# Kernel tuning notes

Hardware: AMD Instinct MI355X
Metric: run time of the kernel (lower is better)

The kernel has to match this reference:

```python
import jax, jax.numpy as jnp
import numpy as np

EPS_NUMER = 1e-8   # numerator init in original code
EPS_D2 = 1e-12     # guard sqrt(0) on the (unused) diagonal


def setup_inputs() -> dict:
    key = jax.random.key(0)
    k0, k1, k2, k3 = jax.random.split(key, 4)
    B, T, C, H, W, D, NC = 128, 128, 3, 32, 32, 1024, 10
    data_t = jax.random.normal(k0, (B, T, 1, C, H, W), jnp.float32)
    responses_t = jax.random.normal(k1, (B, T, NC), jnp.float32)
    teaching_signal_t = jax.random.uniform(k2, (B, T, NC), jnp.float32)
    # feature extractor = single linear layer; scaled so distances are moderate
    W_fe = jax.random.normal(k3, (C * H * W, D), jnp.float32) / np.float32(np.sqrt(C * H * W))
    b_fe = jnp.zeros((D,), jnp.float32)
    c = jnp.ones((1,), jnp.float32)
    gamma = jnp.ones((1,), jnp.float32)
    return dict(responses_t=responses_t, data_t=data_t, teaching_signal_t=teaching_signal_t,
                W_fe=W_fe, b_fe=b_fe, c=c, gamma=gamma)


def reference(responses_t, data_t, teaching_signal_t, W_fe, b_fe, c, gamma):
    B, T = data_t.shape[:2]
    # feature extraction: (B*T, C*H*W) @ (C*H*W, D) -> (B, T, 1, D)
    x = data_t.reshape(B * T, -1)
    feats = (x @ W_fe + b_fe).reshape(B, T, 1, -1)
    f = feats[:, :, 0]                                   # (B, T, D)
    # batched pairwise euclidean distance, then extra .sqrt() as in original
    sq = jnp.sum(f * f, axis=-1)                          # (B, T)
    d2 = sq[:, :, None] + sq[:, None, :] - 2.0 * jnp.einsum('bsd,btd->bst', f, f)
    d2 = jnp.maximum(d2, EPS_D2)
    dist = jnp.sqrt(jnp.sqrt(d2))                         # sqrt(cdist) per original
    sims = jnp.exp(-c[0] * dist)                          # (B, S, T)
    # causal weighted sum: numers[b,t,cls] = eps + sum_{s<t} sims[b,s,t]*teach[b,s,cls]
    causal = jnp.tril(jnp.ones((T, T), sims.dtype), -1).T  # mask[s,t] = 1 if s < t
    numers = EPS_NUMER + jnp.einsum('bst,st,bsc->btc', sims, causal, teaching_signal_t)
    tmp = numers ** gamma[0]
    score = tmp / jnp.sum(tmp, axis=-1, keepdims=True)
    # t == 0 uses raw numers (all EPS_NUMER), not normalized
    score = score.at[:, 0].set(EPS_NUMER)
    responses = score[:, :, None, :]                      # (B, T, 1, NC)
    return responses
```

## Files before the change

kernel.cpp:

```cpp
#include <hip/hip_runtime.h>

typedef short short8 __attribute__((ext_vector_type(8)));
typedef float f32x4 __attribute__((ext_vector_type(4)));
typedef unsigned int uint4v __attribute__((ext_vector_type(4)));

#define EPS_NUMER_F 1e-8f
#define EPS_D2_F 1e-12f

#define BB 128
#define TT 128
#define DD 1024
#define CHW 3072
#define NC 10
#define MM (BB * TT)
#define NT 48

#define GLOAD_LDS16(g, l)                                              \
  __builtin_amdgcn_global_load_lds(                                    \
      (const __attribute__((address_space(1))) void*)(g),              \
      (__attribute__((address_space(3))) void*)(l), 16, 0, 0)

#define DS_READ_B128(dst_, off_) \
  asm volatile("ds_read_b128 %0, %1" : "=v"(dst_) : "v"(off_))
#define DS_WRITE_B128(off_, val_) \
  asm volatile("ds_write_b128 %0, %1" :: "v"(off_), "v"(val_))

#define GLB_LOAD_X4(dst_, voff_, imm_) \
  asm volatile("global_load_dwordx4 %0, %1, %2 offset:" #imm_ \
               : "=v"(dst_) : "v"(voff_), "s"(xbase))

static __device__ __forceinline__ unsigned lds_addr(const void* p) {
  return (unsigned)(unsigned long long)(const __attribute__((address_space(3))) void*)p;
}
static __device__ __forceinline__ unsigned cvt2(float lo, float hi) {
  unsigned r;
  asm("v_cvt_pk_bf16_f32 %0, %1, %2" : "=v"(r) : "v"(lo), "v"(hi));
  return r;
}

static __device__ __forceinline__ short f2bf(float x) {
  unsigned int u = __float_as_uint(x);
  u = (u + 0x7fffu + ((u >> 16) & 1u)) >> 16;
  return (short)u;
}
static __device__ __forceinline__ float bf2f(short x) {
  return __uint_as_float(((unsigned int)(unsigned short)x) << 16);
}

__global__ __launch_bounds__(256) void k_transpose_w(const float* __restrict__ W,
                                                     short* __restrict__ Wt) {
  __shared__ float tile[32][33];
  const int n0 = blockIdx.x * 32;
  const int k0 = blockIdx.y * 32;
  const int tx = threadIdx.x & 31;
  const int ty = threadIdx.x >> 5;
#pragma unroll
  for (int i = 0; i < 32; i += 8)
    tile[ty + i][tx] = W[(size_t)(k0 + ty + i) * DD + (n0 + tx)];
  __syncthreads();
#pragma unroll
  for (int i = 0; i < 32; i += 8)
    Wt[(size_t)(n0 + ty + i) * CHW + (k0 + tx)] = f2bf(tile[tx][ty + i]);
}

__global__ __launch_bounds__(512, 2) void k_gemm_8ph(const float* __restrict__ X,
                                                     const short* __restrict__ Wt,
                                                     const float* __restrict__ bias,
                                                     short* __restrict__ F) {
  __shared__ short As[2][256 * 64];
  __shared__ short Bs[2][256 * 64];

  const int bid = blockIdx.x;
  const int id = (bid & 7) * 32 + (bid >> 3);
  const int bm = (id >> 2) << 8;
  const int bn = (id & 3) << 8;

  const int tid = threadIdx.x;
  const int lane = tid & 63;
  const int wid = tid >> 6;
  const int wr = wid >> 2;
  const int wc = wid & 3;

  const int srow = lane >> 3;
  const int sslot = (lane & 7) ^ (lane >> 3);
  const short* bSrc = Wt + (size_t)(bn + srow) * CHW + sslot * 8;

#define STAGE_B_HALF(T_, h_) do {                                            \
    int base_ = (h_) * 128 + wid * 8;                                        \
    GLOAD_LDS16(bSrc + (size_t)(base_) * CHW + (T_) * 64,                    \
                &Bs[(T_) & 1][(base_) * 64]);                                \
    GLOAD_LDS16(bSrc + (size_t)(base_ + 64) * CHW + (T_) * 64,              \
                &Bs[(T_) & 1][(base_ + 64) * 64]);                           \
  } while (0)

  const int arow_st = wid * 16 + (lane >> 3);
  const unsigned long long xbase = (unsigned long long)X;
  unsigned voff[4];
#pragma unroll
  for (int h = 0; h < 2; ++h)
#pragma unroll
    for (int j = 0; j < 2; ++j)
      voff[h * 2 + j] = (unsigned)(((bm + h * 128 + j * 8 + arow_st) * (size_t)CHW
                                    + (lane & 7) * 8) * 4);
  const unsigned aposb = (unsigned)(((lane & 7) ^ (lane >> 3)) * 16);

  f32x4 ra[4], rb[4];

#define LOAD_A_H0() do {                                                     \
    GLB_LOAD_X4(ra[0], voff[0], 0);  GLB_LOAD_X4(ra[1], voff[0], 16);        \
    GLB_LOAD_X4(ra[2], voff[1], 0);  GLB_LOAD_X4(ra[3], voff[1], 16);        \
  } while (0)
#define LOAD_A_H1() do {                                                     \
    GLB_LOAD_X4(rb[0], voff[2], 0);  GLB_LOAD_X4(rb[1], voff[2], 16);        \
    GLB_LOAD_X4(rb[2], voff[3], 0);  GLB_LOAD_X4(rb[3], voff[3], 16);        \
  } while (0)
#define ADV_A() do { voff[0] += 256; voff[1] += 256; voff[2] += 256; voff[3] += 256; } while (0)
#define WRITE_A_HALF(T_, h_, d_) do {                                        \
    unsigned ad_ = aWrBase + (((T_) & 1) ? 32768u : 0u) + (h_) * 16384u;     \
    uint4v w0_, w1_;                                                         \
    w0_.x = cvt2(d_[0].x, d_[0].y); w0_.y = cvt2(d_[0].z, d_[0].w);          \
    w0_.z = cvt2(d_[1].x, d_[1].y); w0_.w = cvt2(d_[1].z, d_[1].w);          \
    DS_WRITE_B128(ad_, w0_);                                                 \
    w1_.x = cvt2(d_[2].x, d_[2].y); w1_.y = cvt2(d_[2].z, d_[2].w);          \
    w1_.z = cvt2(d_[3].x, d_[3].y); w1_.w = cvt2(d_[3].z, d_[3].w);          \
    DS_WRITE_B128(ad_ + 1024u, w1_);                                         \
  } while (0)

  const int fr = lane & 15;
  const int sl = lane >> 4;
  const int slotk0 = (0 + sl) ^ (lane & 7);
  const int slotk1 = (4 + sl) ^ (lane & 7);
  const int arow = wr * 128 + fr;
  const int brow = wc * 64 + fr;

  const unsigned aBase0 = lds_addr(&As[0][0]);
  const unsigned bBase0 = lds_addr(&Bs[0][0]);
  const unsigned aWrBase = aBase0 + (unsigned)(arow_st * 128) + aposb;

  f32x4 acc[8][4] = {};

  LOAD_A_H0();
  LOAD_A_H1();
  ADV_A();
  STAGE_B_HALF(0, 0); STAGE_B_HALF(0, 1);
  STAGE_B_HALF(1, 0); STAGE_B_HALF(1, 1);
  __builtin_amdgcn_sched_barrier(0);
  asm volatile("s_waitcnt vmcnt(4)");
  __builtin_amdgcn_sched_barrier(0);
  WRITE_A_HALF(0, 0, ra);
  WRITE_A_HALF(0, 1, rb);
  asm volatile("s_waitcnt lgkmcnt(0)");
  __builtin_amdgcn_sched_barrier(0);
  __builtin_amdgcn_s_barrier();

  for (int T = 0; T < NT; ++T) {
    const unsigned ab = aBase0 + ((T & 1) ? 32768u : 0u);
    const unsigned bb = bBase0 + ((T & 1) ? 32768u : 0u);
    short8 bf_[8];
    short8 aq[4];

#define READ_AQ(q_) do {                                                       \
      DS_READ_B128(aq[0], ab + (unsigned)((arow + (2*(q_))    *16)*128 + slotk0*16)); \
      DS_READ_B128(aq[1], ab + (unsigned)((arow + (2*(q_))    *16)*128 + slotk1*16)); \
      DS_READ_B128(aq[2], ab + (unsigned)((arow + (2*(q_) + 1)*16)*128 + slotk0*16)); \
      DS_READ_B128(aq[3], ab + (unsigned)((arow + (2*(q_) + 1)*16)*128 + slotk1*16)); \
    } while (0)
#define MFMA16(q_) do {                                                      \
      _Pragma("unroll")                                                      \
      for (int m2 = 0; m2 < 2; ++m2)                                         \
        _Pragma("unroll")                                                    \
        for (int ks = 0; ks < 2; ++ks)                                       \
          _Pragma("unroll")                                                  \
          for (int ni = 0; ni < 4; ++ni)                                     \
            acc[2*(q_)+m2][ni] = __builtin_amdgcn_mfma_f32_16x16x32_bf16(    \
                aq[m2*2+ks], bf_[ni*2+ks], acc[2*(q_)+m2][ni], 0, 0, 0);     \
    } while (0)
#define PHASE_MID() do {                                                     \
      __builtin_amdgcn_sched_barrier(0);                                     \
      __builtin_amdgcn_s_barrier();                                          \
      asm volatile("s_waitcnt lgkmcnt(0)");                                  \
      __builtin_amdgcn_sched_barrier(0);                                     \
    } while (0)

    if (T + 1 < NT) LOAD_A_H0();
#pragma unroll
    for (int ni = 0; ni < 4; ++ni) {
      DS_READ_B128(bf_[ni * 2 + 0], bb + (unsigned)((brow + ni * 16) * 128 + slotk0 * 16));
      DS_READ_B128(bf_[ni * 2 + 1], bb + (unsigned)((brow + ni * 16) * 128 + slotk1 * 16));
    }
    READ_AQ(0);
    PHASE_MID();
    __builtin_amdgcn_s_setprio(1);
    MFMA16(0);
    __builtin_amdgcn_s_setprio(0);
    __builtin_amdgcn_s_barrier();

    if (T + 1 < NT) LOAD_A_H1();
    ADV_A();
    READ_AQ(1);
    PHASE_MID();
    __builtin_amdgcn_s_setprio(1);
    MFMA16(1);
    __builtin_amdgcn_s_setprio(0);
    __builtin_amdgcn_s_barrier();

    READ_AQ(2);
    if (T + 2 < NT) {
      STAGE_B_HALF(T + 2, 0);
      __builtin_amdgcn_sched_barrier(0);
      asm volatile("s_waitcnt vmcnt(6)");
      __builtin_amdgcn_sched_barrier(0);
    } else if (T + 1 < NT) {
      __builtin_amdgcn_sched_barrier(0);
      asm volatile("s_waitcnt vmcnt(4)");
      __builtin_amdgcn_sched_barrier(0);
    }
    if (T + 1 < NT) WRITE_A_HALF(T + 1, 0, ra);
    PHASE_MID();
    __builtin_amdgcn_s_setprio(1);
    MFMA16(2);
    __builtin_amdgcn_s_setprio(0);
    __builtin_amdgcn_s_barrier();

    READ_AQ(3);
    if (T + 2 < NT) {
      STAGE_B_HALF(T + 2, 1);
      __builtin_amdgcn_sched_barrier(0);
      asm volatile("s_waitcnt vmcnt(4)");
      __builtin_amdgcn_sched_barrier(0);
    } else if (T + 1 < NT) {
      __builtin_amdgcn_sched_barrier(0);
      asm volatile("s_waitcnt vmcnt(0)");
      __builtin_amdgcn_sched_barrier(0);
    }
    if (T + 1 < NT) WRITE_A_HALF(T + 1, 1, rb);
    PHASE_MID();
    __builtin_amdgcn_s_setprio(1);
    MFMA16(3);
    __builtin_amdgcn_s_setprio(0);
    __builtin_amdgcn_s_barrier();
  }

  const int cc = lane & 15;
  const int crr = sl << 2;
#pragma unroll
  for (int ni = 0; ni < 4; ++ni) {
    int col = bn + wc * 64 + ni * 16 + cc;
    float bv = bias[col];
#pragma unroll
    for (int mi = 0; mi < 8; ++mi) {
      int row0 = bm + wr * 128 + mi * 16 + crr;
#pragma unroll
      for (int q = 0; q < 4; ++q)
        F[(size_t)(row0 + q) * DD + col] = f2bf(acc[mi][ni][q] + bv);
    }
  }
#undef READ_AQ
#undef MFMA16
#undef PHASE_MID
#undef STAGE_B_HALF
}

__global__ __launch_bounds__(256) void k_batch_sims(const short* __restrict__ F,
                                                    const float* __restrict__ teach,
                                                    const float* __restrict__ cptr,
                                                    const float* __restrict__ gptr,
                                                    float* __restrict__ out) {
  __shared__ short ftile[128][40];
  __shared__ float simsT[64][129];
  __shared__ float sqv[128];
  __shared__ float sqp[256];
  __shared__ float teach_s[128][NC];
  __shared__ float numer[64][NC];
  __shared__ float rsum[64];

  const int b = blockIdx.x >> 1;
  const int half = blockIdx.x & 1;
  const int tid = threadIdx.x;
  const int lane = tid & 63;
  const int w = tid >> 6;
  const size_t fbase = (size_t)b * TT * DD;

  for (int idx = tid; idx < TT * NC; idx += 256)
    teach_s[idx / NC][idx % NC] = teach[(size_t)b * TT * NC + idx];

  {
    int row = tid >> 1;
    int kh = (tid & 1) << 9;
    const short* fp = F + fbase + (size_t)row * DD + kh;
    float s = 0.f;
    for (int k = 0; k < 512; k += 8) {
      short8 v = *reinterpret_cast<const short8*>(fp + k);
#pragma unroll
      for (int j = 0; j < 8; ++j) { float x = bf2f(v[j]); s += x * x; }
    }
    sqp[tid] = s;
  }
  __syncthreads();
  if (tid < 128) sqv[tid] = sqp[2 * tid] + sqp[2 * tid + 1];
  __syncthreads();

  f32x4 acc[2][4] = {};
  const int fr = lane & 15;
  const int fk = (lane >> 4) << 3;
  for (int k0 = 0; k0 < DD; k0 += 32) {
#pragma unroll
    for (int i = 0; i < 2; ++i) {
      int idx = tid + (i << 8);
      int row = idx >> 2;
      int kc = (idx & 3) << 3;
      short8 v = *reinterpret_cast<const short8*>(F + fbase + (size_t)row * DD + (k0 + kc));
      *reinterpret_cast<short8*>(&ftile[row][kc]) = v;
    }
    __syncthreads();
    short8 af[2], bfv[4];
#pragma unroll
    for (int mi = 0; mi < 2; ++mi)
      af[mi] = *reinterpret_cast<const short8*>(&ftile[w * 32 + mi * 16 + fr][fk]);
#pragma unroll
    for (int ni = 0; ni < 4; ++ni)
      bfv[ni] = *reinterpret_cast<const short8*>(&ftile[half * 64 + ni * 16 + fr][fk]);
#pragma unroll
    for (int mi = 0; mi < 2; ++mi)
#pragma unroll
      for (int ni = 0; ni < 4; ++ni)
        acc[mi][ni] = __builtin_amdgcn_mfma_f32_16x16x32_bf16(af[mi], bfv[ni], acc[mi][ni], 0, 0, 0);
    __syncthreads();
  }

  const float c0 = cptr[0];
  const int cc = lane & 15;
  const int crr = (lane >> 4) << 2;
#pragma unroll
  for (int mi = 0; mi < 2; ++mi) {
#pragma unroll
    for (int ni = 0; ni < 4; ++ni) {
#pragma unroll
      for (int q = 0; q < 4; ++q) {
        int s_g = w * 32 + mi * 16 + crr + q;
        int tl = ni * 16 + cc;
        int t_g = half * 64 + tl;
        float g = acc[mi][ni][q];
        float d2 = sqv[s_g] + sqv[t_g] - 2.0f * g;
        d2 = fmaxf(d2, EPS_D2_F);
        float dist = sqrtf(sqrtf(d2));
        simsT[tl][s_g] = (s_g < t_g) ? expf(-c0 * dist) : 0.0f;
      }
    }
  }
  __syncthreads();

  const float gam = gptr[0];
  for (int idx = tid; idx < 64 * NC; idx += 256) {
    int tl = idx / NC, c = idx % NC;
    float s = 0.f;
#pragma unroll 4
    for (int si = 0; si < TT; ++si)
      s += simsT[tl][si] * teach_s[si][c];
    float v = EPS_NUMER_F + s;
    numer[tl][c] = (gam == 1.0f) ? v : powf(v, gam);
  }
  __syncthreads();
  if (tid < 64) {
    float s = 0.f;
#pragma unroll
    for (int c = 0; c < NC; ++c) s += numer[tid][c];
    rsum[tid] = s;
  }
  __syncthreads();
  for (int idx = tid; idx < 64 * NC; idx += 256) {
    int tl = idx / NC, c = idx % NC;
    int t_g = half * 64 + tl;
    float v = numer[tl][c] / rsum[tl];
    if (t_g == 0) v = EPS_NUMER_F;
    out[(size_t)b * TT * NC + (size_t)t_g * NC + c] = v;
  }
}

extern "C" void kernel_launch(void* const* d_in, const int* in_sizes, int n_in,
                              void* d_out, int out_size, void* d_ws, size_t ws_size,
                              hipStream_t stream) {
  const float* data = (const float*)d_in[1];
  const float* teach = (const float*)d_in[2];
  const float* Wfe = (const float*)d_in[3];
  const float* bfe = (const float*)d_in[4];
  const float* cp = (const float*)d_in[5];
  const float* gp = (const float*)d_in[6];
  float* outp = (float*)d_out;

  char* ws = (char*)d_ws;
  short* Wt = (short*)ws;
  short* F = (short*)(ws + (size_t)8 * 1024 * 1024);

  k_transpose_w<<<dim3(DD / 32, CHW / 32), 256, 0, stream>>>(Wfe, Wt);
  k_gemm_8ph<<<dim3((MM / 256) * (DD / 256)), 512, 0, stream>>>(data, Wt, bfe, F);
  k_batch_sims<<<dim3(BB * 2), 256, 0, stream>>>(F, teach, cp, gp, outp);
}
```

Baseline: 146.7 us.

## Double-buffer A fragments in registers to overlap LDS reads with MFMA

The feature-extraction GEMM main loop now keeps two register sets for A fragments (even and odd quarters). Each quarter's LDS reads are issued before the previous quarter's MFMAs, and the full lgkmcnt(0) waits become partial lgkmcnt waits. This is meant to hide LDS read latency behind matrix-core work instead of stalling at every phase boundary. In exchange it needs about 16 more VGPRs and relies on exact counts of outstanding LDS operations, which makes the code more fragile to ordering changes.

```diff
diff --git a/kernel.cpp b/kernel.cpp
--- a/kernel.cpp
+++ b/kernel.cpp
@@ -24,10 +24,10 @@
   asm volatile("ds_read_b128 %0, %1" : "=v"(dst_) : "v"(off_))
 #define DS_WRITE_B128(off_, val_) \
   asm volatile("ds_write_b128 %0, %1" :: "v"(off_), "v"(val_))
-
 #define GLB_LOAD_X4(dst_, voff_, imm_) \
   asm volatile("global_load_dwordx4 %0, %1, %2 offset:" #imm_ \
                : "=v"(dst_) : "v"(voff_), "s"(xbase))
+#define SCHED_FENCE() __builtin_amdgcn_sched_barrier(0)
 
 static __device__ __forceinline__ unsigned lds_addr(const void* p) {
   return (unsigned)(unsigned long long)(const __attribute__((address_space(3))) void*)p;
@@ -137,107 +137,125 @@
   const unsigned bBase0 = lds_addr(&Bs[0][0]);
   const unsigned aWrBase = aBase0 + (unsigned)(arow_st * 128) + aposb;
 
+  short8 bf_[8];
+  short8 aqE[4], aqO[4];
   f32x4 acc[8][4] = {};
+
+#define READ_B8(bb_) do {                                                    \
+    _Pragma("unroll")                                                        \
+    for (int ni = 0; ni < 4; ++ni) {                                         \
+      DS_READ_B128(bf_[ni * 2 + 0], (bb_) + (unsigned)((brow + ni * 16) * 128 + slotk0 * 16)); \
+      DS_READ_B128(bf_[ni * 2 + 1], (bb_) + (unsigned)((brow + ni * 16) * 128 + slotk1 * 16)); \
+    }                                                                        \
+  } while (0)
+#define READ_AQ(set_, q_, ab_) do {                                          \
+    DS_READ_B128(set_[0], (ab_) + (unsigned)((arow + (2*(q_))    *16)*128 + slotk0*16)); \
+    DS_READ_B128(set_[1], (ab_) + (unsigned)((arow + (2*(q_))    *16)*128 + slotk1*16)); \
+    DS_READ_B128(set_[2], (ab_) + (unsigned)((arow + (2*(q_) + 1)*16)*128 + slotk0*16)); \
+    DS_READ_B128(set_[3], (ab_) + (unsigned)((arow + (2*(q_) + 1)*16)*128 + slotk1*16)); \
+  } while (0)
+#define MFMA16(q_, set_) do {                                                \
+    _Pragma("unroll")                                                        \
+    for (int m2 = 0; m2 < 2; ++m2)                                           \
+      _Pragma("unroll")                                                      \
+      for (int ks = 0; ks < 2; ++ks)                                         \
+        _Pragma("unroll")                                                    \
+        for (int ni = 0; ni < 4; ++ni)                                       \
+          acc[2*(q_)+m2][ni] = __builtin_amdgcn_mfma_f32_16x16x32_bf16(      \
+              set_[m2*2+ks], bf_[ni*2+ks], acc[2*(q_)+m2][ni], 0, 0, 0);     \
+  } while (0)
 
   LOAD_A_H0();
   LOAD_A_H1();
   ADV_A();
   STAGE_B_HALF(0, 0); STAGE_B_HALF(0, 1);
   STAGE_B_HALF(1, 0); STAGE_B_HALF(1, 1);
-  __builtin_amdgcn_sched_barrier(0);
+  SCHED_FENCE();
   asm volatile("s_waitcnt vmcnt(4)");
-  __builtin_amdgcn_sched_barrier(0);
+  SCHED_FENCE();
   WRITE_A_HALF(0, 0, ra);
   WRITE_A_HALF(0, 1, rb);
   asm volatile("s_waitcnt lgkmcnt(0)");
-  __builtin_amdgcn_sched_barrier(0);
+  SCHED_FENCE();
   __builtin_amdgcn_s_barrier();
 
   for (int T = 0; T < NT; ++T) {
     const unsigned ab = aBase0 + ((T & 1) ? 32768u : 0u);
     const unsigned bb = bBase0 + ((T & 1) ? 32768u : 0u);
-    short8 bf_[8];
-    short8 aq[4];
-
-#define READ_AQ(q_) do {                                                       \
-      DS_READ_B128(aq[0], ab + (unsigned)((arow + (2*(q_))    *16)*128 + slotk0*16)); \
-      DS_READ_B128(aq[1], ab + (unsigned)((arow + (2*(q_))    *16)*128 + slotk1*16)); \
-      DS_READ_B128(aq[2], ab + (unsigned)((arow + (2*(q_) + 1)*16)*128 + slotk0*16)); \
-      DS_READ_B128(aq[3], ab + (unsigned)((arow + (2*(q_) + 1)*16)*128 + slotk1*16)); \
-    } while (0)
-#define MFMA16(q_) do {                                                      \
-      _Pragma("unroll")                                                      \
-      for (int m2 = 0; m2 < 2; ++m2)                                         \
-        _Pragma("unroll")                                                    \
-        for (int ks = 0; ks < 2; ++ks)                                       \
-          _Pragma("unroll")                                                  \
-          for (int ni = 0; ni < 4; ++ni)                                     \
-            acc[2*(q_)+m2][ni] = __builtin_amdgcn_mfma_f32_16x16x32_bf16(    \
-                aq[m2*2+ks], bf_[ni*2+ks], acc[2*(q_)+m2][ni], 0, 0, 0);     \
-    } while (0)
-#define PHASE_MID() do {                                                     \
-      __builtin_amdgcn_sched_barrier(0);                                     \
-      __builtin_amdgcn_s_barrier();                                          \
-      asm volatile("s_waitcnt lgkmcnt(0)");                                  \
-      __builtin_amdgcn_sched_barrier(0);                                     \
-    } while (0)
-
+
+    READ_B8(bb);
+    READ_AQ(aqE, 0, ab);
+    READ_AQ(aqO, 1, ab);
     if (T + 1 < NT) LOAD_A_H0();
-#pragma unroll
-    for (int ni = 0; ni < 4; ++ni) {
-      DS_READ_B128(bf_[ni * 2 + 0], bb + (unsigned)((brow + ni * 16) * 128 + slotk0 * 16));
-      DS_READ_B128(bf_[ni * 2 + 1], bb + (unsigned)((brow + ni * 16) * 128 + slotk1 * 16));
-    }
-    READ_AQ(0);
-    PHASE_MID();
+    SCHED_FENCE();
+    __builtin_amdgcn_s_barrier();
+    asm volatile("s_waitcnt lgkmcnt(4)");
+    SCHED_FENCE();
     __builtin_amdgcn_s_setprio(1);
-    MFMA16(0);
+    MFMA16(0, aqE);
     __builtin_amdgcn_s_setprio(0);
-    __builtin_amdgcn_s_barrier();
-
+    SCHED_FENCE();
+    __builtin_amdgcn_s_barrier();
+
+    READ_AQ(aqE, 2, ab);
     if (T + 1 < NT) LOAD_A_H1();
     ADV_A();
-    READ_AQ(1);
-    PHASE_MID();
+    SCHED_FENCE();
+    __builtin_amdgcn_s_barrier();
+    asm volatile("s_waitcnt lgkmcnt(4)");
+    SCHED_FENCE();
     __builtin_amdgcn_s_setprio(1);
-    MFMA16(1);
+    MFMA16(1, aqO);
     __builtin_amdgcn_s_setprio(0);
-    __builtin_amdgcn_s_barrier();
-
-    READ_AQ(2);
+    SCHED_FENCE();
+    __builtin_amdgcn_s_barrier();
+
     if (T + 2 < NT) {
       STAGE_B_HALF(T + 2, 0);
-      __builtin_amdgcn_sched_barrier(0);
+      SCHED_FENCE();
       asm volatile("s_waitcnt vmcnt(6)");
-      __builtin_amdgcn_sched_barrier(0);
+      SCHED_FENCE();
     } else if (T + 1 < NT) {
-      __builtin_amdgcn_sched_barrier(0);
+      SCHED_FENCE();
       asm volatile("s_waitcnt vmcnt(4)");
-      __builtin_amdgcn_sched_barrier(0);
+      SCHED_FENCE();
     }
     if (T + 1 < NT) WRITE_A_HALF(T + 1, 0, ra);
-    PHASE_MID();
+    READ_AQ(aqO, 3, ab);
+    SCHED_FENCE();
+    __builtin_amdgcn_s_barrier();
+    asm volatile("s_waitcnt lgkmcnt(4)");
+    SCHED_FENCE();
     __builtin_amdgcn_s_setprio(1);
-    MFMA16(2);
+    MFMA16(2, aqE);
     __builtin_amdgcn_s_setprio(0);
-    __builtin_amdgcn_s_barrier();
-
-    READ_AQ(3);
+    SCHED_FENCE();
+    __builtin_amdgcn_s_barrier();
+
     if (T + 2 < NT) {
       STAGE_B_HALF(T + 2, 1);
-      __builtin_amdgcn_sched_barrier(0);
+      SCHED_FENCE();
       asm volatile("s_waitcnt vmcnt(4)");
-      __builtin_amdgcn_sched_barrier(0);
+      SCHED_FENCE();
     } else if (T + 1 < NT) {
-      __builtin_amdgcn_sched_barrier(0);
+      SCHED_FENCE();
       asm volatile("s_waitcnt vmcnt(0)");
-      __builtin_amdgcn_sched_barrier(0);
+      SCHED_FENCE();
     }
     if (T + 1 < NT) WRITE_A_HALF(T + 1, 1, rb);
-    PHASE_MID();
+    SCHED_FENCE();
+    __builtin_amdgcn_s_barrier();
+    if (T + 1 < NT) {
+      asm volatile("s_waitcnt lgkmcnt(2)");
+    } else {
+      asm volatile("s_waitcnt lgkmcnt(0)");
+    }
+    SCHED_FENCE();
     __builtin_amdgcn_s_setprio(1);
-    MFMA16(3);
+    MFMA16(3, aqO);
     __builtin_amdgcn_s_setprio(0);
+    asm volatile("s_waitcnt lgkmcnt(0)");
+    SCHED_FENCE();
     __builtin_amdgcn_s_barrier();
   }
 
@@ -255,9 +273,9 @@
         F[(size_t)(row0 + q) * DD + col] = f2bf(acc[mi][ni][q] + bv);
     }
   }
+#undef READ_B8
 #undef READ_AQ
 #undef MFMA16
-#undef PHASE_MID
 #undef STAGE_B_HALF
 }
 
```

Measured after the change: 186.8 us. 1.27x slower.
